# Optimization experiments

Measured on AMD Instinct MI355X. Metric: run time of the kernel, lower is better.

Reference implementation:

```python
import jax, jax.numpy as jnp
import numpy as np

HOURS = 24
SU, SL, TU, TL = 100.0, 0.0, 100.0, 0.0
N, M, L, E = 32, 128, 128, 128
T_DIM, U_DIM, L_DIM = 25, 2000, 10000


def setup_inputs() -> dict:
    key = jax.random.key(0)
    ks = jax.random.split(key, 18)
    s = 0.02
    full_seq = jax.random.randint(ks[0], (N, M), 1, L_DIM)
    time_seq = jax.random.randint(ks[1], (N, M), 1, 720)
    user = jax.random.randint(ks[2], (N,), 1, U_DIM)
    posneg = jax.random.randint(ks[3], (N, L), 1, L_DIM)
    traj_len = jax.random.randint(ks[4], (N,), 1, M + 1)
    mat1 = jax.random.uniform(ks[5], (N, M, M, 2), dtype=jnp.float32) * 100.0
    mat2 = jax.random.uniform(ks[6], (N, M, L), dtype=jnp.float32) * 100.0
    vec = jax.random.uniform(ks[7], (N, M), dtype=jnp.float32) * 100.0
    def tab(k, n):  # embedding table with padding_idx=0 zeroed
        return (jax.random.normal(k, (n, E), dtype=jnp.float32) * s).at[0].set(0.0)
    emb_t = tab(ks[8], T_DIM)
    emb_u = tab(ks[9], U_DIM)
    emb_loc = tab(ks[10], L_DIM)
    emb_sl = tab(ks[11], 2)
    emb_su = tab(ks[12], 2)
    emb_tl = tab(ks[13], 2)
    emb_tu = tab(ks[14], 2)
    Wq = jax.random.normal(ks[15], (E, E), dtype=jnp.float32) * s
    Wk = jax.random.normal(ks[16], (E, E), dtype=jnp.float32) * s
    Wv = jax.random.normal(ks[17], (E, E), dtype=jnp.float32) * s
    return dict(full_seq=full_seq, time_seq=time_seq, user=user, posneg=posneg,
                traj_len=traj_len, mat1=mat1, mat2=mat2, vec=vec,
                emb_t=emb_t, emb_u=emb_u, emb_loc=emb_loc,
                emb_sl=emb_sl, emb_su=emb_su, emb_tl=emb_tl, emb_tu=emb_tu,
                Wq=Wq, Wk=Wk, Wv=Wv)


def _interval(e_l, e_u, d, lo, hi):
    # (e_l*(hi-d) + e_u*(d-lo)) / (hi-lo); e_* are [...,E], d is [...]
    return (e_l * (hi - d)[..., None] + e_u * (d - lo)[..., None]) / (hi - lo)


def reference(full_seq, time_seq, user, posneg, traj_len, mat1, mat2, vec,
              emb_t, emb_u, emb_loc, emb_sl, emb_su, emb_tl, emb_tu, Wq, Wk, Wv):
    n, m = full_seq.shape
    tim = (time_seq - 1) % HOURS + 1
    joint = emb_t[tim] + emb_loc[full_seq] + emb_u[user][:, None, :]  # [N,M,E]

    # --- stage 1: self-attention with spatiotemporal relative bias ---
    delta_s, delta_t = mat1[..., 0], mat1[..., 1]  # [N,M,M]
    valid = (jnp.arange(m)[None, :] < traj_len[:, None]).astype(jnp.int32)  # [N,M]
    mask2d = valid[:, None, :] * valid[:, :, None]  # [N,M,M] in {0,1}
    delta = (_interval(emb_sl[mask2d], emb_su[mask2d], delta_s, SL, SU)
             + _interval(emb_tl[mask2d], emb_tu[mask2d], delta_t, TL, TU)).sum(-1)
    fmask = mask2d.astype(joint.dtype)
    q = joint @ Wq.T
    k = joint @ Wk.T
    v = joint @ Wv.T
    attn = jax.nn.softmax(jnp.einsum('bme,bne->bmn', q, k) + delta, axis=-1) * fmask
    self_attn = jnp.einsum('bmn,bne->bme', attn, v)  # [N,M,E]

    # --- stage 2: candidate attention ---
    mask1 = valid[:, :, None]  # [N,M,1]
    sp = _interval(emb_sl[mask1], emb_su[mask1], mat2, SL, SU)            # [N,M,L,E]
    tm = _interval(emb_tl[mask1], emb_tu[mask1], vec[:, :, None], TL, TU)  # [N,M,1,E]
    self_delta = jnp.swapaxes((sp + tm).sum(-1), -1, -2)  # [N,L,M]
    cand = emb_loc[posneg]  # [N,L,E]
    attn2 = jnp.einsum('ble,bme->blm', cand, self_attn) * self_delta
    return attn2.sum(-1)  # [N,L]
```

## Files before the change

### kernel.cpp

```cpp
#include <hip/hip_runtime.h>
#include <hip/hip_bf16.h>

#define HOURS 24
#define NB 32
#define MM 128
#define EE 128

typedef short bf16x8 __attribute__((ext_vector_type(8)));
typedef float f32x4 __attribute__((ext_vector_type(4)));

__device__ __forceinline__ unsigned short f2bfu(float f) {
    __hip_bfloat16 h = __float2bfloat16(f);
    return __builtin_bit_cast(unsigned short, h);
}
__device__ __forceinline__ unsigned int pack2(float a, float b) {
    return (unsigned int)f2bfu(a) | ((unsigned int)f2bfu(b) << 16);
}
__device__ __forceinline__ int swz8(int row, int unit) {
    return row * 128 + (((unit ^ (row & 7)) & 15) << 3);
}

__global__ __launch_bounds__(256) void k_qkv(
    const int* __restrict__ time_seq, const int* __restrict__ full_seq,
    const int* __restrict__ user,
    const float* __restrict__ emb_t, const float* __restrict__ emb_u,
    const float* __restrict__ emb_loc,
    const float* __restrict__ Wq, const float* __restrict__ Wk, const float* __restrict__ Wv,
    short* __restrict__ qws, short* __restrict__ kws, short* __restrict__ vtws)
{
    __shared__ alignas(16) short Wl[128 * 128];
    __shared__ alignas(16) short Jl[64 * 128];
    int b = blockIdx.y;
    int which = blockIdx.x >> 1;
    int half = blockIdx.x & 1;
    int m0 = half * 64;
    int tid = threadIdx.x;
    const float* W = (which == 0) ? Wq : (which == 1) ? Wk : Wv;

    const float4* W4 = (const float4*)W;
#pragma unroll
    for (int it = 0; it < 16; ++it) {
        int i4 = it * 256 + tid;
        float4 v = W4[i4];
        int n = i4 >> 5;
        int e = (i4 & 31) << 2;
        uint2 pk;
        pk.x = pack2(v.x, v.y);
        pk.y = pack2(v.z, v.w);
        *(uint2*)&Wl[swz8(n, e >> 3) + (e & 7)] = pk;
    }
    int uid = user[b];
    const float4* Eu4 = (const float4*)(emb_u + (size_t)uid * 128);
#pragma unroll
    for (int it = 0; it < 8; ++it) {
        int i4 = it * 256 + tid;
        int mm = i4 >> 5;
        int e = (i4 & 31) << 2;
        int m = m0 + mm;
        int t = time_seq[b * MM + m];
        int tim = (t - 1) % HOURS + 1;
        int loc = full_seq[b * MM + m];
        float4 a = ((const float4*)(emb_t + (size_t)tim * 128))[e >> 2];
        float4 c = ((const float4*)(emb_loc + (size_t)loc * 128))[e >> 2];
        float4 u = Eu4[e >> 2];
        uint2 pk;
        pk.x = pack2(a.x + c.x + u.x, a.y + c.y + u.y);
        pk.y = pack2(a.z + c.z + u.z, a.w + c.w + u.w);
        *(uint2*)&Jl[swz8(mm, e >> 3) + (e & 7)] = pk;
    }
    __syncthreads();

    int l = tid & 63, w = tid >> 6;
    int lr = l & 15, lg = l >> 4;

    if (which < 2) {
        bf16x8 af[2][4];
#pragma unroll
        for (int nt = 0; nt < 2; ++nt) {
            int n = (2 * w + nt) * 16 + lr;
#pragma unroll
            for (int kf = 0; kf < 4; ++kf)
                af[nt][kf] = *(const bf16x8*)&Wl[swz8(n, kf * 4 + lg)];
        }
        f32x4 acc[2][4];
#pragma unroll
        for (int nt = 0; nt < 2; ++nt)
#pragma unroll
            for (int mt = 0; mt < 4; ++mt) acc[nt][mt] = (f32x4){0.f, 0.f, 0.f, 0.f};
#pragma unroll
        for (int mt = 0; mt < 4; ++mt) {
            int m = mt * 16 + lr;
            bf16x8 bf[4];
#pragma unroll
            for (int kf = 0; kf < 4; ++kf)
                bf[kf] = *(const bf16x8*)&Jl[swz8(m, kf * 4 + lg)];
#pragma unroll
            for (int nt = 0; nt < 2; ++nt)
#pragma unroll
                for (int kf = 0; kf < 4; ++kf)
                    acc[nt][mt] = __builtin_amdgcn_mfma_f32_16x16x32_bf16(af[nt][kf], bf[kf], acc[nt][mt], 0, 0, 0);
        }
        short* outp = (which == 0) ? qws : kws;
#pragma unroll
        for (int nt = 0; nt < 2; ++nt)
#pragma unroll
            for (int mt = 0; mt < 4; ++mt) {
                int mg = m0 + mt * 16 + lr;
                int n0 = (2 * w + nt) * 16 + lg * 4;
                f32x4 a = acc[nt][mt];
                uint2 pk;
                pk.x = pack2(a[0], a[1]);
                pk.y = pack2(a[2], a[3]);
                *(uint2*)&outp[(size_t)(b * MM + mg) * EE + n0] = pk;
            }
    } else {
        bf16x8 bfr[2][4];
#pragma unroll
        for (int nt = 0; nt < 2; ++nt) {
            int n = (2 * w + nt) * 16 + lr;
#pragma unroll
            for (int kf = 0; kf < 4; ++kf)
                bfr[nt][kf] = *(const bf16x8*)&Wl[swz8(n, kf * 4 + lg)];
        }
        f32x4 acc[4][2];
#pragma unroll
        for (int mt = 0; mt < 4; ++mt)
#pragma unroll
            for (int nt = 0; nt < 2; ++nt) acc[mt][nt] = (f32x4){0.f, 0.f, 0.f, 0.f};
#pragma unroll
        for (int mt = 0; mt < 4; ++mt) {
            int m = mt * 16 + lr;
            bf16x8 af[4];
#pragma unroll
            for (int kf = 0; kf < 4; ++kf)
                af[kf] = *(const bf16x8*)&Jl[swz8(m, kf * 4 + lg)];
#pragma unroll
            for (int nt = 0; nt < 2; ++nt)
#pragma unroll
                for (int kf = 0; kf < 4; ++kf)
                    acc[mt][nt] = __builtin_amdgcn_mfma_f32_16x16x32_bf16(af[kf], bfr[nt][kf], acc[mt][nt], 0, 0, 0);
        }
#pragma unroll
        for (int mt = 0; mt < 4; ++mt)
#pragma unroll
            for (int nt = 0; nt < 2; ++nt) {
                int ng = (2 * w + nt) * 16 + lr;
                int mp = m0 + mt * 16 + lg * 4;
                f32x4 a = acc[mt][nt];
                uint2 pk;
                pk.x = pack2(a[0], a[1]);
                pk.y = pack2(a[2], a[3]);
                *(uint2*)&vtws[(size_t)(b * MM + ng) * MM + mp] = pk;
            }
    }
}

__global__ __launch_bounds__(256) void k_attn(
    const short* __restrict__ qws, const short* __restrict__ kws,
    const short* __restrict__ vtws,
    const float* __restrict__ mat1, const int* __restrict__ traj_len,
    const float* __restrict__ esl, const float* __restrict__ esu,
    const float* __restrict__ etl, const float* __restrict__ etu,
    short* __restrict__ saws)
{
    __shared__ alignas(16) short Kl[128 * 128];
    __shared__ alignas(16) short VTl[128 * 128];
    __shared__ alignas(16) short Pl[16 * 128];
    __shared__ alignas(16) float Sl[16][132];
    __shared__ float coef[8];

    int b = blockIdx.y;
    int chunk = blockIdx.x;
    int i0 = chunk * 16;
    int tid = threadIdx.x;
    int l = tid & 63, w = tid >> 6;
    int lr = l & 15, lg = l >> 4;
    int tl = traj_len[b];

    {
        const float* tb[4] = {esl, esu, etl, etu};
#pragma unroll
        for (int s = 0; s < 2; ++s) {
            int c = 2 * w + s;
            const float* t = tb[c >> 1];
            float v = t[(c & 1) * 128 + l] + t[(c & 1) * 128 + 64 + l];
#pragma unroll
            for (int off = 32; off >= 1; off >>= 1) v += __shfl_xor(v, off, 64);
            if (l == 0) coef[c] = v;
        }
    }
    const uint4* K4 = (const uint4*)(kws + (size_t)b * MM * EE);
    const uint4* VT4 = (const uint4*)(vtws + (size_t)b * MM * MM);
#pragma unroll
    for (int it = 0; it < 8; ++it) {
        int U = it * 256 + tid;
        int r = U >> 4, u = U & 15;
        *(uint4*)&Kl[swz8(r, u)] = K4[U];
    }
#pragma unroll
    for (int it = 0; it < 8; ++it) {
        int U = it * 256 + tid;
        int r = U >> 4, u = U & 15;
        *(uint4*)&VTl[swz8(r, u)] = VT4[U];
    }
    bf16x8 qf[4];
#pragma unroll
    for (int kf = 0; kf < 4; ++kf)
        qf[kf] = *(const bf16x8*)&qws[(size_t)(b * MM + i0 + lr) * EE + kf * 32 + lg * 8];
    __syncthreads();

    f32x4 accs[2];
#pragma unroll
    for (int t2 = 0; t2 < 2; ++t2) accs[t2] = (f32x4){0.f, 0.f, 0.f, 0.f};
#pragma unroll
    for (int t2 = 0; t2 < 2; ++t2) {
        int j = (2 * w + t2) * 16 + lr;
#pragma unroll
        for (int kf = 0; kf < 4; ++kf) {
            bf16x8 bf = *(const bf16x8*)&Kl[swz8(j, kf * 4 + lg)];
            accs[t2] = __builtin_amdgcn_mfma_f32_16x16x32_bf16(qf[kf], bf, accs[t2], 0, 0, 0);
        }
    }
#pragma unroll
    for (int t2 = 0; t2 < 2; ++t2) {
        int jc = (2 * w + t2) * 16 + lr;
#pragma unroll
        for (int r = 0; r < 4; ++r) Sl[lg * 4 + r][jc] = accs[t2][r];
    }
    __syncthreads();

    {
        int r16 = tid >> 4, u = tid & 15;
        int j0 = u * 8;
        int i = i0 + r16;
        int mi = (i < tl) ? 1 : 0;
        float c0_1 = coef[1] + coef[5];
        float c1_1 = (coef[3] - coef[1]) * 0.01f;
        float c2_1 = (coef[7] - coef[5]) * 0.01f;
        float c0_0 = coef[0] + coef[4];
        float c1_0 = (coef[2] - coef[0]) * 0.01f;
        float c2_0 = (coef[6] - coef[4]) * 0.01f;
        float4 s01 = *(float4*)&Sl[r16][j0];
        float4 s23 = *(float4*)&Sl[r16][j0 + 4];
        float sv[8] = {s01.x, s01.y, s01.z, s01.w, s23.x, s23.y, s23.z, s23.w};
        const float4* m14 = (const float4*)(mat1 + (size_t)(b * MM + i) * MM * 2 + j0 * 2);
        float4 d0 = m14[0], d1 = m14[1], d2 = m14[2], d3 = m14[3];
        float ds[8] = {d0.x, d0.z, d1.x, d1.z, d2.x, d2.z, d3.x, d3.z};
        float dt[8] = {d0.y, d0.w, d1.y, d1.w, d2.y, d2.w, d3.y, d3.w};
        float lgv[8];
        int mk[8];
#pragma unroll
        for (int jj = 0; jj < 8; ++jj) {
            int j = j0 + jj;
            mk[jj] = mi & ((j < tl) ? 1 : 0);
            float cc0 = mk[jj] ? c0_1 : c0_0;
            float cc1 = mk[jj] ? c1_1 : c1_0;
            float cc2 = mk[jj] ? c2_1 : c2_0;
            lgv[jj] = sv[jj] + cc0 + cc1 * ds[jj] + cc2 * dt[jj];
        }
        float mx = lgv[0];
#pragma unroll
        for (int jj = 1; jj < 8; ++jj) mx = fmaxf(mx, lgv[jj]);
#pragma unroll
        for (int off = 8; off >= 1; off >>= 1) mx = fmaxf(mx, __shfl_xor(mx, off, 64));
        float ee[8], sum = 0.f;
#pragma unroll
        for (int jj = 0; jj < 8; ++jj) { ee[jj] = __expf(lgv[jj] - mx); sum += ee[jj]; }
#pragma unroll
        for (int off = 8; off >= 1; off >>= 1) sum += __shfl_xor(sum, off, 64);
        float inv = 1.0f / sum;
        float p[8];
#pragma unroll
        for (int jj = 0; jj < 8; ++jj) p[jj] = ee[jj] * inv * (float)mk[jj];
        uint4 pk;
        pk.x = pack2(p[0], p[1]);
        pk.y = pack2(p[2], p[3]);
        pk.z = pack2(p[4], p[5]);
        pk.w = pack2(p[6], p[7]);
        *(uint4*)&Pl[swz8(r16, u)] = pk;
    }
    __syncthreads();

    bf16x8 bp[4];
#pragma unroll
    for (int kf = 0; kf < 4; ++kf)
        bp[kf] = *(const bf16x8*)&Pl[swz8(lr, kf * 4 + lg)];
    f32x4 accv[2];
#pragma unroll
    for (int t2 = 0; t2 < 2; ++t2) accv[t2] = (f32x4){0.f, 0.f, 0.f, 0.f};
#pragma unroll
    for (int t2 = 0; t2 < 2; ++t2) {
        int e = (2 * w + t2) * 16 + lr;
#pragma unroll
        for (int kf = 0; kf < 4; ++kf) {
            bf16x8 af = *(const bf16x8*)&VTl[swz8(e, kf * 4 + lg)];
            accv[t2] = __builtin_amdgcn_mfma_f32_16x16x32_bf16(af, bp[kf], accv[t2], 0, 0, 0);
        }
    }
#pragma unroll
    for (int t2 = 0; t2 < 2; ++t2) {
        int ig = i0 + lr;
        int e0 = (2 * w + t2) * 16 + lg * 4;
        f32x4 a = accv[t2];
        uint2 pk;
        pk.x = pack2(a[0], a[1]);
        pk.y = pack2(a[2], a[3]);
        *(uint2*)&saws[(size_t)(b * MM + ig) * EE + e0] = pk;
    }
}

__global__ __launch_bounds__(256) void k_final(
    const short* __restrict__ saws, const int* __restrict__ posneg,
    const float* __restrict__ emb_loc, const float* __restrict__ mat2,
    const float* __restrict__ vecg, const int* __restrict__ traj_len,
    const float* __restrict__ esl, const float* __restrict__ esu,
    const float* __restrict__ etl, const float* __restrict__ etu,
    float* __restrict__ outp)
{
    __shared__ alignas(16) short SAl[128 * 128];
    __shared__ alignas(16) short CAl[32 * 128];
    __shared__ alignas(16) float M2l[128 * 36];
    __shared__ float TMS[128];
    __shared__ float BSV[128];
    __shared__ float PART[2][32];
    __shared__ float coef[8];

    int b = blockIdx.y;
    int l0 = blockIdx.x * 32;
    int tid = threadIdx.x;
    int l = tid & 63, w = tid >> 6;
    int lr = l & 15, lg = l >> 4;
    int tl = traj_len[b];

    {
        const float* tb[4] = {esl, esu, etl, etu};
#pragma unroll
        for (int s = 0; s < 2; ++s) {
            int c = 2 * w + s;
            const float* t = tb[c >> 1];
            float v = t[(c & 1) * 128 + l] + t[(c & 1) * 128 + 64 + l];
#pragma unroll
            for (int off = 32; off >= 1; off >>= 1) v += __shfl_xor(v, off, 64);
            if (l == 0) coef[c] = v;
        }
    }
    const uint4* SA4 = (const uint4*)(saws + (size_t)b * MM * EE);
#pragma unroll
    for (int it = 0; it < 8; ++it) {
        int U = it * 256 + tid;
        int r = U >> 4, u = U & 15;
        *(uint4*)&SAl[swz8(r, u)] = SA4[U];
    }
#pragma unroll
    for (int it = 0; it < 4; ++it) {
        int i4 = it * 256 + tid;
        int lrow = i4 >> 5;
        int e = (i4 & 31) << 2;
        int p = posneg[b * MM + l0 + lrow];
        float4 v = ((const float4*)(emb_loc + (size_t)p * 128))[e >> 2];
        uint2 pk;
        pk.x = pack2(v.x, v.y);
        pk.y = pack2(v.z, v.w);
        *(uint2*)&CAl[swz8(lrow, e >> 3) + (e & 7)] = pk;
    }
#pragma unroll
    for (int it = 0; it < 4; ++it) {
        int i4 = it * 256 + tid;
        int m = i4 >> 3;
        int c = (i4 & 7) << 2;
        float4 v = ((const float4*)(mat2 + (size_t)(b * MM + m) * MM + l0))[c >> 2];
        *(float4*)&M2l[m * 36 + c] = v;
    }
    __syncthreads();

    if (tid < 128) {
        int vv = (tid < tl) ? 1 : 0;
        float ssl = vv ? coef[1] : coef[0];
        float ssu = vv ? coef[3] : coef[2];
        float stl = vv ? coef[5] : coef[4];
        float stu = vv ? coef[7] : coef[6];
        TMS[tid] = ssl + stl + (stu - stl) * 0.01f * vecg[b * MM + tid];
        BSV[tid] = (ssu - ssl) * 0.01f;
    }

    int ltile = w & 1, mhalf = w >> 1;
    bf16x8 ca[4];
#pragma unroll
    for (int kf = 0; kf < 4; ++kf)
        ca[kf] = *(const bf16x8*)&CAl[swz8(ltile * 16 + lr, kf * 4 + lg)];
    f32x4 acc[4];
#pragma unroll
    for (int mt = 0; mt < 4; ++mt) acc[mt] = (f32x4){0.f, 0.f, 0.f, 0.f};
#pragma unroll
    for (int mt = 0; mt < 4; ++mt) {
        int m = (mhalf * 4 + mt) * 16 + lr;
#pragma unroll
        for (int kf = 0; kf < 4; ++kf) {
            bf16x8 bf = *(const bf16x8*)&SAl[swz8(m, kf * 4 + lg)];
            acc[mt] = __builtin_amdgcn_mfma_f32_16x16x32_bf16(ca[kf], bf, acc[mt], 0, 0, 0);
        }
    }
    __syncthreads();

#pragma unroll
    for (int r = 0; r < 4; ++r) {
        int lrel = ltile * 16 + lg * 4 + r;
        float vs = 0.f;
#pragma unroll
        for (int mt = 0; mt < 4; ++mt) {
            int m = (mhalf * 4 + mt) * 16 + lr;
            vs += acc[mt][r] * (TMS[m] + BSV[m] * M2l[m * 36 + lrel]);
        }
#pragma unroll
        for (int off = 8; off >= 1; off >>= 1) vs += __shfl_xor(vs, off, 64);
        if (lr == 0) PART[mhalf][lrel] = vs;
    }
    __syncthreads();
    if (tid < 32) outp[b * MM + l0 + tid] = PART[0][tid] + PART[1][tid];
}

extern "C" void kernel_launch(void* const* d_in, const int* in_sizes, int n_in,
                              void* d_out, int out_size, void* d_ws, size_t ws_size,
                              hipStream_t stream) {
    const int* full_seq = (const int*)d_in[0];
    const int* time_seq = (const int*)d_in[1];
    const int* user     = (const int*)d_in[2];
    const int* posneg   = (const int*)d_in[3];
    const int* traj_len = (const int*)d_in[4];
    const float* mat1   = (const float*)d_in[5];
    const float* mat2   = (const float*)d_in[6];
    const float* vec    = (const float*)d_in[7];
    const float* emb_t  = (const float*)d_in[8];
    const float* emb_u  = (const float*)d_in[9];
    const float* emb_loc= (const float*)d_in[10];
    const float* emb_sl = (const float*)d_in[11];
    const float* emb_su = (const float*)d_in[12];
    const float* emb_tl = (const float*)d_in[13];
    const float* emb_tu = (const float*)d_in[14];
    const float* Wq     = (const float*)d_in[15];
    const float* Wk     = (const float*)d_in[16];
    const float* Wv     = (const float*)d_in[17];

    short* qws  = (short*)d_ws;
    short* kws  = qws + (size_t)NB * MM * EE;
    short* vtws = kws + (size_t)NB * MM * EE;
    short* saws = vtws + (size_t)NB * MM * EE;

    k_qkv<<<dim3(6, 32), 256, 0, stream>>>(time_seq, full_seq, user,
                                           emb_t, emb_u, emb_loc,
                                           Wq, Wk, Wv, qws, kws, vtws);
    k_attn<<<dim3(8, 32), 256, 0, stream>>>(qws, kws, vtws, mat1, traj_len,
                                            emb_sl, emb_su, emb_tl, emb_tu, saws);
    k_final<<<dim3(4, 32), 256, 0, stream>>>(saws, posneg, emb_loc, mat2, vec,
                                             traj_len, emb_sl, emb_su, emb_tl, emb_tu,
                                             (float*)d_out);
}
```

Before: 24.17 us.

## Fuse QKV, attention and candidate stages into one kernel per batch half

Replaces the three-kernel pipeline (QKV projection, self-attention, candidate attention) with a single 1024-thread kernel that runs per (batch, half of query rows) and keeps Q, K, V^T, probabilities and self-attention output in shared memory. Global workspace round trips and two kernel launches are removed. Each half block recomputes full K and V for its batch, and the two halves' partial candidate sums are combined with atomicAdd into an output zeroed by a memset. This duplicates some projection work, cuts the grid to 64 blocks, and uses large LDS per block.

```diff
diff --git a/kernel.cpp b/kernel.cpp
--- a/kernel.cpp
+++ b/kernel.cpp
@@ -2,7 +2,6 @@
 #include <hip/hip_bf16.h>
 
 #define HOURS 24
-#define NB 32
 #define MM 128
 #define EE 128
 
@@ -19,231 +18,188 @@
 __device__ __forceinline__ int swz8(int row, int unit) {
     return row * 128 + (((unit ^ (row & 7)) & 15) << 3);
 }
-
-__global__ __launch_bounds__(256) void k_qkv(
-    const int* __restrict__ time_seq, const int* __restrict__ full_seq,
-    const int* __restrict__ user,
+__device__ __forceinline__ bf16x8 load_w_frag(const float* base) {
+    float4 x = *(const float4*)base;
+    float4 y = *(const float4*)(base + 4);
+    union { unsigned int u[4]; bf16x8 v; } r;
+    r.u[0] = pack2(x.x, x.y); r.u[1] = pack2(x.z, x.w);
+    r.u[2] = pack2(y.x, y.y); r.u[3] = pack2(y.z, y.w);
+    return r.v;
+}
+
+#define MFMA(a, b, c) __builtin_amdgcn_mfma_f32_16x16x32_bf16(a, b, c, 0, 0, 0)
+
+__global__ __launch_bounds__(1024) void k_fused(
+    const int* __restrict__ full_seq, const int* __restrict__ time_seq,
+    const int* __restrict__ user, const int* __restrict__ posneg,
+    const int* __restrict__ traj_len,
+    const float* __restrict__ mat1, const float* __restrict__ mat2,
+    const float* __restrict__ vecg,
     const float* __restrict__ emb_t, const float* __restrict__ emb_u,
     const float* __restrict__ emb_loc,
-    const float* __restrict__ Wq, const float* __restrict__ Wk, const float* __restrict__ Wv,
-    short* __restrict__ qws, short* __restrict__ kws, short* __restrict__ vtws)
-{
-    __shared__ alignas(16) short Wl[128 * 128];
-    __shared__ alignas(16) short Jl[64 * 128];
-    int b = blockIdx.y;
-    int which = blockIdx.x >> 1;
-    int half = blockIdx.x & 1;
-    int m0 = half * 64;
-    int tid = threadIdx.x;
-    const float* W = (which == 0) ? Wq : (which == 1) ? Wk : Wv;
-
-    const float4* W4 = (const float4*)W;
-#pragma unroll
-    for (int it = 0; it < 16; ++it) {
-        int i4 = it * 256 + tid;
-        float4 v = W4[i4];
-        int n = i4 >> 5;
-        int e = (i4 & 31) << 2;
-        uint2 pk;
-        pk.x = pack2(v.x, v.y);
-        pk.y = pack2(v.z, v.w);
-        *(uint2*)&Wl[swz8(n, e >> 3) + (e & 7)] = pk;
-    }
-    int uid = user[b];
-    const float4* Eu4 = (const float4*)(emb_u + (size_t)uid * 128);
-#pragma unroll
-    for (int it = 0; it < 8; ++it) {
-        int i4 = it * 256 + tid;
-        int mm = i4 >> 5;
-        int e = (i4 & 31) << 2;
-        int m = m0 + mm;
-        int t = time_seq[b * MM + m];
-        int tim = (t - 1) % HOURS + 1;
-        int loc = full_seq[b * MM + m];
-        float4 a = ((const float4*)(emb_t + (size_t)tim * 128))[e >> 2];
-        float4 c = ((const float4*)(emb_loc + (size_t)loc * 128))[e >> 2];
-        float4 u = Eu4[e >> 2];
-        uint2 pk;
-        pk.x = pack2(a.x + c.x + u.x, a.y + c.y + u.y);
-        pk.y = pack2(a.z + c.z + u.z, a.w + c.w + u.w);
-        *(uint2*)&Jl[swz8(mm, e >> 3) + (e & 7)] = pk;
-    }
-    __syncthreads();
-
-    int l = tid & 63, w = tid >> 6;
-    int lr = l & 15, lg = l >> 4;
-
-    if (which < 2) {
-        bf16x8 af[2][4];
-#pragma unroll
-        for (int nt = 0; nt < 2; ++nt) {
-            int n = (2 * w + nt) * 16 + lr;
-#pragma unroll
-            for (int kf = 0; kf < 4; ++kf)
-                af[nt][kf] = *(const bf16x8*)&Wl[swz8(n, kf * 4 + lg)];
-        }
-        f32x4 acc[2][4];
-#pragma unroll
-        for (int nt = 0; nt < 2; ++nt)
-#pragma unroll
-            for (int mt = 0; mt < 4; ++mt) acc[nt][mt] = (f32x4){0.f, 0.f, 0.f, 0.f};
-#pragma unroll
-        for (int mt = 0; mt < 4; ++mt) {
-            int m = mt * 16 + lr;
-            bf16x8 bf[4];
-#pragma unroll
-            for (int kf = 0; kf < 4; ++kf)
-                bf[kf] = *(const bf16x8*)&Jl[swz8(m, kf * 4 + lg)];
-#pragma unroll
-            for (int nt = 0; nt < 2; ++nt)
-#pragma unroll
-                for (int kf = 0; kf < 4; ++kf)
-                    acc[nt][mt] = __builtin_amdgcn_mfma_f32_16x16x32_bf16(af[nt][kf], bf[kf], acc[nt][mt], 0, 0, 0);
-        }
-        short* outp = (which == 0) ? qws : kws;
-#pragma unroll
-        for (int nt = 0; nt < 2; ++nt)
-#pragma unroll
-            for (int mt = 0; mt < 4; ++mt) {
-                int mg = m0 + mt * 16 + lr;
-                int n0 = (2 * w + nt) * 16 + lg * 4;
-                f32x4 a = acc[nt][mt];
-                uint2 pk;
-                pk.x = pack2(a[0], a[1]);
-                pk.y = pack2(a[2], a[3]);
-                *(uint2*)&outp[(size_t)(b * MM + mg) * EE + n0] = pk;
-            }
-    } else {
-        bf16x8 bfr[2][4];
-#pragma unroll
-        for (int nt = 0; nt < 2; ++nt) {
-            int n = (2 * w + nt) * 16 + lr;
-#pragma unroll
-            for (int kf = 0; kf < 4; ++kf)
-                bfr[nt][kf] = *(const bf16x8*)&Wl[swz8(n, kf * 4 + lg)];
-        }
-        f32x4 acc[4][2];
-#pragma unroll
-        for (int mt = 0; mt < 4; ++mt)
-#pragma unroll
-            for (int nt = 0; nt < 2; ++nt) acc[mt][nt] = (f32x4){0.f, 0.f, 0.f, 0.f};
-#pragma unroll
-        for (int mt = 0; mt < 4; ++mt) {
-            int m = mt * 16 + lr;
-            bf16x8 af[4];
-#pragma unroll
-            for (int kf = 0; kf < 4; ++kf)
-                af[kf] = *(const bf16x8*)&Jl[swz8(m, kf * 4 + lg)];
-#pragma unroll
-            for (int nt = 0; nt < 2; ++nt)
-#pragma unroll
-                for (int kf = 0; kf < 4; ++kf)
-                    acc[mt][nt] = __builtin_amdgcn_mfma_f32_16x16x32_bf16(af[kf], bfr[nt][kf], acc[mt][nt], 0, 0, 0);
-        }
-#pragma unroll
-        for (int mt = 0; mt < 4; ++mt)
-#pragma unroll
-            for (int nt = 0; nt < 2; ++nt) {
-                int ng = (2 * w + nt) * 16 + lr;
-                int mp = m0 + mt * 16 + lg * 4;
-                f32x4 a = acc[mt][nt];
-                uint2 pk;
-                pk.x = pack2(a[0], a[1]);
-                pk.y = pack2(a[2], a[3]);
-                *(uint2*)&vtws[(size_t)(b * MM + ng) * MM + mp] = pk;
-            }
-    }
-}
-
-__global__ __launch_bounds__(256) void k_attn(
-    const short* __restrict__ qws, const short* __restrict__ kws,
-    const short* __restrict__ vtws,
-    const float* __restrict__ mat1, const int* __restrict__ traj_len,
     const float* __restrict__ esl, const float* __restrict__ esu,
     const float* __restrict__ etl, const float* __restrict__ etu,
-    short* __restrict__ saws)
+    const float* __restrict__ Wq, const float* __restrict__ Wk,
+    const float* __restrict__ Wv,
+    float* __restrict__ outp)
 {
-    __shared__ alignas(16) short Kl[128 * 128];
-    __shared__ alignas(16) short VTl[128 * 128];
-    __shared__ alignas(16) short Pl[16 * 128];
-    __shared__ alignas(16) float Sl[16][132];
-    __shared__ float coef[8];
-
-    int b = blockIdx.y;
-    int chunk = blockIdx.x;
-    int i0 = chunk * 16;
+    __shared__ alignas(16) short A_s[16896];
+    __shared__ alignas(16) short B_s[17408];
+    __shared__ alignas(16) short C_s[16384];
+    __shared__ alignas(16) short D_s[8192];
+    __shared__ alignas(16) short E_s[8192];
+    __shared__ float tms[64], bsv[64], coef[8];
+
+    int bid = blockIdx.x;
+    int b = bid >> 1, half = bid & 1;
+    int i0base = half * 64;
     int tid = threadIdx.x;
-    int l = tid & 63, w = tid >> 6;
+    int w = tid >> 6, l = tid & 63;
     int lr = l & 15, lg = l >> 4;
     int tl = traj_len[b];
 
-    {
-        const float* tb[4] = {esl, esu, etl, etu};
-#pragma unroll
-        for (int s = 0; s < 2; ++s) {
-            int c = 2 * w + s;
-            const float* t = tb[c >> 1];
-            float v = t[(c & 1) * 128 + l] + t[(c & 1) * 128 + 64 + l];
-#pragma unroll
-            for (int off = 32; off >= 1; off >>= 1) v += __shfl_xor(v, off, 64);
-            if (l == 0) coef[c] = v;
-        }
-    }
-    const uint4* K4 = (const uint4*)(kws + (size_t)b * MM * EE);
-    const uint4* VT4 = (const uint4*)(vtws + (size_t)b * MM * MM);
-#pragma unroll
-    for (int it = 0; it < 8; ++it) {
-        int U = it * 256 + tid;
-        int r = U >> 4, u = U & 15;
-        *(uint4*)&Kl[swz8(r, u)] = K4[U];
-    }
-#pragma unroll
-    for (int it = 0; it < 8; ++it) {
-        int U = it * 256 + tid;
-        int r = U >> 4, u = U & 15;
-        *(uint4*)&VTl[swz8(r, u)] = VT4[U];
-    }
-    bf16x8 qf[4];
-#pragma unroll
-    for (int kf = 0; kf < 4; ++kf)
-        qf[kf] = *(const bf16x8*)&qws[(size_t)(b * MM + i0 + lr) * EE + kf * 32 + lg * 8];
-    __syncthreads();
-
-    f32x4 accs[2];
-#pragma unroll
-    for (int t2 = 0; t2 < 2; ++t2) accs[t2] = (f32x4){0.f, 0.f, 0.f, 0.f};
-#pragma unroll
-    for (int t2 = 0; t2 < 2; ++t2) {
-        int j = (2 * w + t2) * 16 + lr;
-#pragma unroll
-        for (int kf = 0; kf < 4; ++kf) {
-            bf16x8 bf = *(const bf16x8*)&Kl[swz8(j, kf * 4 + lg)];
-            accs[t2] = __builtin_amdgcn_mfma_f32_16x16x32_bf16(qf[kf], bf, accs[t2], 0, 0, 0);
-        }
-    }
-#pragma unroll
-    for (int t2 = 0; t2 < 2; ++t2) {
-        int jc = (2 * w + t2) * 16 + lr;
-#pragma unroll
-        for (int r = 0; r < 4; ++r) Sl[lg * 4 + r][jc] = accs[t2][r];
-    }
-    __syncthreads();
-
-    {
-        int r16 = tid >> 4, u = tid & 15;
-        int j0 = u * 8;
-        int i = i0 + r16;
-        int mi = (i < tl) ? 1 : 0;
+    if (w >= 8) {
+        int c = w - 8;
+        const float* t = (c < 2) ? esl : (c < 4) ? esu : (c < 6) ? etl : etu;
+        int row = c & 1;
+        float v = t[row * 128 + l] + t[row * 128 + 64 + l];
+#pragma unroll
+        for (int off = 32; off >= 1; off >>= 1) v += __shfl_xor(v, off, 64);
+        if (l == 0) coef[c] = v;
+    }
+    {
+        int uid = user[b];
+        const float4* Eu4 = (const float4*)(emb_u + (size_t)uid * 128);
+#pragma unroll
+        for (int it = 0; it < 4; ++it) {
+            int u = it * 1024 + tid;
+            int mm = u >> 5;
+            int fq = u & 31;
+            int t = time_seq[b * MM + mm];
+            int tim = (t - 1) % HOURS + 1;
+            int loc = full_seq[b * MM + mm];
+            float4 a = ((const float4*)(emb_t + (size_t)tim * 128))[fq];
+            float4 c = ((const float4*)(emb_loc + (size_t)loc * 128))[fq];
+            float4 uu = Eu4[fq];
+            uint2 pk;
+            pk.x = pack2(a.x + c.x + uu.x, a.y + c.y + uu.y);
+            pk.y = pack2(a.z + c.z + uu.z, a.w + c.w + uu.w);
+            *(uint2*)&A_s[swz8(mm, fq >> 1) + (fq & 1) * 4] = pk;
+        }
+    }
+    __syncthreads();
+
+    if (w < 8) {
+        bf16x8 af[4];
+#pragma unroll
+        for (int kf = 0; kf < 4; ++kf)
+            af[kf] = load_w_frag(Wk + (size_t)(w * 16 + lr) * 128 + kf * 32 + lg * 8);
+        f32x4 acc[8];
+#pragma unroll
+        for (int mt = 0; mt < 8; ++mt) acc[mt] = (f32x4){0.f, 0.f, 0.f, 0.f};
+#pragma unroll
+        for (int mt = 0; mt < 8; ++mt)
+#pragma unroll
+            for (int kf = 0; kf < 4; ++kf) {
+                bf16x8 bf = *(const bf16x8*)&A_s[swz8(mt * 16 + lr, kf * 4 + lg)];
+                acc[mt] = MFMA(af[kf], bf, acc[mt]);
+            }
+        int n0 = w * 16 + lg * 4;
+#pragma unroll
+        for (int mt = 0; mt < 8; ++mt) {
+            int m = mt * 16 + lr;
+            uint2 pk;
+            pk.x = pack2(acc[mt][0], acc[mt][1]);
+            pk.y = pack2(acc[mt][2], acc[mt][3]);
+            *(uint2*)&B_s[swz8(m, n0 >> 3) + (n0 & 7)] = pk;
+        }
+    } else {
+        int w8 = w - 8;
+        bf16x8 aj[4];
+#pragma unroll
+        for (int kf = 0; kf < 4; ++kf)
+            aj[kf] = *(const bf16x8*)&A_s[swz8(w8 * 16 + lr, kf * 4 + lg)];
+#pragma unroll
+        for (int nt = 0; nt < 8; ++nt) {
+            f32x4 acc = (f32x4){0.f, 0.f, 0.f, 0.f};
+#pragma unroll
+            for (int kf = 0; kf < 4; ++kf) {
+                bf16x8 bw = load_w_frag(Wv + (size_t)(nt * 16 + lr) * 128 + kf * 32 + lg * 8);
+                acc = MFMA(aj[kf], bw, acc);
+            }
+            int n = nt * 16 + lr;
+#pragma unroll
+            for (int r = 0; r < 4; ++r) {
+                int m = w8 * 16 + lg * 4 + r;
+                C_s[swz8(n, m >> 3) + (m & 7)] = (short)f2bfu(acc[r]);
+            }
+        }
+    }
+    {
+        int nt = w & 7;
+        int mtb = (w < 8) ? 0 : 2;
+        bf16x8 aq[4];
+#pragma unroll
+        for (int kf = 0; kf < 4; ++kf)
+            aq[kf] = load_w_frag(Wq + (size_t)(nt * 16 + lr) * 128 + kf * 32 + lg * 8);
+#pragma unroll
+        for (int mi = 0; mi < 2; ++mi) {
+            int mt = mtb + mi;
+            f32x4 acc = (f32x4){0.f, 0.f, 0.f, 0.f};
+#pragma unroll
+            for (int kf = 0; kf < 4; ++kf) {
+                bf16x8 bf = *(const bf16x8*)&A_s[swz8(i0base + mt * 16 + lr, kf * 4 + lg)];
+                acc = MFMA(aq[kf], bf, acc);
+            }
+            int iloc = mt * 16 + lr;
+            int n0 = nt * 16 + lg * 4;
+            uint2 pk;
+            pk.x = pack2(acc[0], acc[1]);
+            pk.y = pack2(acc[2], acc[3]);
+            *(uint2*)&D_s[swz8(iloc, n0 >> 3) + (n0 & 7)] = pk;
+        }
+    }
+    __syncthreads();
+
+    float* Sf = (float*)A_s;
+    {
+        int chunk = w >> 2, sub = w & 3;
+        bf16x8 qf[4];
+#pragma unroll
+        for (int kf = 0; kf < 4; ++kf)
+            qf[kf] = *(const bf16x8*)&D_s[swz8(chunk * 16 + lr, kf * 4 + lg)];
+#pragma unroll
+        for (int t2 = 0; t2 < 2; ++t2) {
+            int jt = sub * 2 + t2;
+            f32x4 acc = (f32x4){0.f, 0.f, 0.f, 0.f};
+#pragma unroll
+            for (int kf = 0; kf < 4; ++kf) {
+                bf16x8 bf = *(const bf16x8*)&B_s[swz8(jt * 16 + lr, kf * 4 + lg)];
+                acc = MFMA(qf[kf], bf, acc);
+            }
+#pragma unroll
+            for (int r = 0; r < 4; ++r)
+                Sf[chunk * 2112 + (lg * 4 + r) * 132 + jt * 16 + lr] = acc[r];
+        }
+    }
+    __syncthreads();
+
+    {
+        int chunk = tid >> 8, t256 = tid & 255;
+        int r16 = t256 >> 4, u = t256 & 15, j0 = u * 8;
+        int ig = i0base + chunk * 16 + r16;
+        int mi = (ig < tl) ? 1 : 0;
         float c0_1 = coef[1] + coef[5];
         float c1_1 = (coef[3] - coef[1]) * 0.01f;
         float c2_1 = (coef[7] - coef[5]) * 0.01f;
         float c0_0 = coef[0] + coef[4];
         float c1_0 = (coef[2] - coef[0]) * 0.01f;
         float c2_0 = (coef[6] - coef[4]) * 0.01f;
-        float4 s01 = *(float4*)&Sl[r16][j0];
-        float4 s23 = *(float4*)&Sl[r16][j0 + 4];
+        const float* sb = &Sf[chunk * 2112 + r16 * 132 + j0];
+        float4 s01 = *(const float4*)sb;
+        float4 s23 = *(const float4*)(sb + 4);
         float sv[8] = {s01.x, s01.y, s01.z, s01.w, s23.x, s23.y, s23.z, s23.w};
-        const float4* m14 = (const float4*)(mat1 + (size_t)(b * MM + i) * MM * 2 + j0 * 2);
+        const float4* m14 = (const float4*)(mat1 + ((size_t)(b * MM + ig) * MM + j0) * 2);
         float4 d0 = m14[0], d1 = m14[1], d2 = m14[2], d3 = m14[3];
         float ds[8] = {d0.x, d0.z, d1.x, d1.z, d2.x, d2.z, d3.x, d3.z};
         float dt[8] = {d0.y, d0.w, d1.y, d1.w, d2.y, d2.w, d3.y, d3.w};
@@ -269,154 +225,109 @@
 #pragma unroll
         for (int off = 8; off >= 1; off >>= 1) sum += __shfl_xor(sum, off, 64);
         float inv = 1.0f / sum;
-        float p[8];
-#pragma unroll
-        for (int jj = 0; jj < 8; ++jj) p[jj] = ee[jj] * inv * (float)mk[jj];
         uint4 pk;
-        pk.x = pack2(p[0], p[1]);
-        pk.y = pack2(p[2], p[3]);
-        pk.z = pack2(p[4], p[5]);
-        pk.w = pack2(p[6], p[7]);
-        *(uint4*)&Pl[swz8(r16, u)] = pk;
-    }
-    __syncthreads();
-
-    bf16x8 bp[4];
-#pragma unroll
-    for (int kf = 0; kf < 4; ++kf)
-        bp[kf] = *(const bf16x8*)&Pl[swz8(lr, kf * 4 + lg)];
-    f32x4 accv[2];
-#pragma unroll
-    for (int t2 = 0; t2 < 2; ++t2) accv[t2] = (f32x4){0.f, 0.f, 0.f, 0.f};
-#pragma unroll
-    for (int t2 = 0; t2 < 2; ++t2) {
-        int e = (2 * w + t2) * 16 + lr;
-#pragma unroll
-        for (int kf = 0; kf < 4; ++kf) {
-            bf16x8 af = *(const bf16x8*)&VTl[swz8(e, kf * 4 + lg)];
-            accv[t2] = __builtin_amdgcn_mfma_f32_16x16x32_bf16(af, bp[kf], accv[t2], 0, 0, 0);
-        }
-    }
-#pragma unroll
-    for (int t2 = 0; t2 < 2; ++t2) {
-        int ig = i0 + lr;
-        int e0 = (2 * w + t2) * 16 + lg * 4;
-        f32x4 a = accv[t2];
-        uint2 pk;
-        pk.x = pack2(a[0], a[1]);
-        pk.y = pack2(a[2], a[3]);
-        *(uint2*)&saws[(size_t)(b * MM + ig) * EE + e0] = pk;
-    }
-}
-
-__global__ __launch_bounds__(256) void k_final(
-    const short* __restrict__ saws, const int* __restrict__ posneg,
-    const float* __restrict__ emb_loc, const float* __restrict__ mat2,
-    const float* __restrict__ vecg, const int* __restrict__ traj_len,
-    const float* __restrict__ esl, const float* __restrict__ esu,
-    const float* __restrict__ etl, const float* __restrict__ etu,
-    float* __restrict__ outp)
-{
-    __shared__ alignas(16) short SAl[128 * 128];
-    __shared__ alignas(16) short CAl[32 * 128];
-    __shared__ alignas(16) float M2l[128 * 36];
-    __shared__ float TMS[128];
-    __shared__ float BSV[128];
-    __shared__ float PART[2][32];
-    __shared__ float coef[8];
-
-    int b = blockIdx.y;
-    int l0 = blockIdx.x * 32;
-    int tid = threadIdx.x;
-    int l = tid & 63, w = tid >> 6;
-    int lr = l & 15, lg = l >> 4;
-    int tl = traj_len[b];
-
-    {
-        const float* tb[4] = {esl, esu, etl, etu};
-#pragma unroll
-        for (int s = 0; s < 2; ++s) {
-            int c = 2 * w + s;
-            const float* t = tb[c >> 1];
-            float v = t[(c & 1) * 128 + l] + t[(c & 1) * 128 + 64 + l];
-#pragma unroll
-            for (int off = 32; off >= 1; off >>= 1) v += __shfl_xor(v, off, 64);
-            if (l == 0) coef[c] = v;
-        }
-    }
-    const uint4* SA4 = (const uint4*)(saws + (size_t)b * MM * EE);
-#pragma unroll
-    for (int it = 0; it < 8; ++it) {
-        int U = it * 256 + tid;
-        int r = U >> 4, u = U & 15;
-        *(uint4*)&SAl[swz8(r, u)] = SA4[U];
-    }
-#pragma unroll
-    for (int it = 0; it < 4; ++it) {
-        int i4 = it * 256 + tid;
-        int lrow = i4 >> 5;
-        int e = (i4 & 31) << 2;
-        int p = posneg[b * MM + l0 + lrow];
-        float4 v = ((const float4*)(emb_loc + (size_t)p * 128))[e >> 2];
-        uint2 pk;
-        pk.x = pack2(v.x, v.y);
-        pk.y = pack2(v.z, v.w);
-        *(uint2*)&CAl[swz8(lrow, e >> 3) + (e & 7)] = pk;
-    }
-#pragma unroll
-    for (int it = 0; it < 4; ++it) {
-        int i4 = it * 256 + tid;
-        int m = i4 >> 3;
-        int c = (i4 & 7) << 2;
-        float4 v = ((const float4*)(mat2 + (size_t)(b * MM + m) * MM + l0))[c >> 2];
-        *(float4*)&M2l[m * 36 + c] = v;
-    }
-    __syncthreads();
-
-    if (tid < 128) {
-        int vv = (tid < tl) ? 1 : 0;
+        pk.x = pack2(ee[0] * inv * mk[0], ee[1] * inv * mk[1]);
+        pk.y = pack2(ee[2] * inv * mk[2], ee[3] * inv * mk[3]);
+        pk.z = pack2(ee[4] * inv * mk[4], ee[5] * inv * mk[5]);
+        pk.w = pack2(ee[6] * inv * mk[6], ee[7] * inv * mk[7]);
+        *(uint4*)&D_s[chunk * 2048 + swz8(r16, u)] = pk;
+    }
+    if (tid < 64) {
+        int mg = i0base + tid;
+        int vv = (mg < tl) ? 1 : 0;
         float ssl = vv ? coef[1] : coef[0];
         float ssu = vv ? coef[3] : coef[2];
         float stl = vv ? coef[5] : coef[4];
         float stu = vv ? coef[7] : coef[6];
-        TMS[tid] = ssl + stl + (stu - stl) * 0.01f * vecg[b * MM + tid];
-        BSV[tid] = (ssu - ssl) * 0.01f;
-    }
-
-    int ltile = w & 1, mhalf = w >> 1;
-    bf16x8 ca[4];
-#pragma unroll
-    for (int kf = 0; kf < 4; ++kf)
-        ca[kf] = *(const bf16x8*)&CAl[swz8(ltile * 16 + lr, kf * 4 + lg)];
-    f32x4 acc[4];
-#pragma unroll
-    for (int mt = 0; mt < 4; ++mt) acc[mt] = (f32x4){0.f, 0.f, 0.f, 0.f};
-#pragma unroll
-    for (int mt = 0; mt < 4; ++mt) {
-        int m = (mhalf * 4 + mt) * 16 + lr;
-#pragma unroll
-        for (int kf = 0; kf < 4; ++kf) {
-            bf16x8 bf = *(const bf16x8*)&SAl[swz8(m, kf * 4 + lg)];
-            acc[mt] = __builtin_amdgcn_mfma_f32_16x16x32_bf16(ca[kf], bf, acc[mt], 0, 0, 0);
-        }
-    }
-    __syncthreads();
-
-#pragma unroll
-    for (int r = 0; r < 4; ++r) {
-        int lrel = ltile * 16 + lg * 4 + r;
-        float vs = 0.f;
-#pragma unroll
-        for (int mt = 0; mt < 4; ++mt) {
-            int m = (mhalf * 4 + mt) * 16 + lr;
-            vs += acc[mt][r] * (TMS[m] + BSV[m] * M2l[m * 36 + lrel]);
-        }
-#pragma unroll
-        for (int off = 8; off >= 1; off >>= 1) vs += __shfl_xor(vs, off, 64);
-        if (lr == 0) PART[mhalf][lrel] = vs;
-    }
-    __syncthreads();
-    if (tid < 32) outp[b * MM + l0 + tid] = PART[0][tid] + PART[1][tid];
+        tms[tid] = ssl + stl + (stu - stl) * 0.01f * vecg[b * MM + mg];
+        bsv[tid] = (ssu - ssl) * 0.01f;
+    }
+    __syncthreads();
+
+    if (w < 8) {
+        int chunk = w >> 1, eh = w & 1;
+        bf16x8 bp[4];
+#pragma unroll
+        for (int kf = 0; kf < 4; ++kf)
+            bp[kf] = *(const bf16x8*)&D_s[chunk * 2048 + swz8(lr, kf * 4 + lg)];
+#pragma unroll
+        for (int e4 = 0; e4 < 4; ++e4) {
+            int et = eh * 4 + e4;
+            f32x4 acc = (f32x4){0.f, 0.f, 0.f, 0.f};
+#pragma unroll
+            for (int kf = 0; kf < 4; ++kf) {
+                bf16x8 af = *(const bf16x8*)&C_s[swz8(et * 16 + lr, kf * 4 + lg)];
+                acc = MFMA(af, bp[kf], acc);
+            }
+            int iloc = chunk * 16 + lr;
+            int e0 = et * 16 + lg * 4;
+            uint2 pk;
+            pk.x = pack2(acc[0], acc[1]);
+            pk.y = pack2(acc[2], acc[3]);
+            *(uint2*)&E_s[swz8(iloc, e0 >> 3) + (e0 & 7)] = pk;
+        }
+    } else {
+        int w8 = w - 8;
+#pragma unroll
+        for (int it = 0; it < 8; ++it) {
+            int u512 = it * 64 + l;
+            int rr = u512 >> 5, fq = u512 & 31;
+            int row = w8 * 16 + rr;
+            int p = posneg[b * MM + row];
+            float4 v = *(const float4*)(emb_loc + (size_t)p * 128 + fq * 4);
+            uint2 pk;
+            pk.x = pack2(v.x, v.y);
+            pk.y = pack2(v.z, v.w);
+            *(uint2*)&A_s[swz8(row, fq >> 1) + (fq & 1) * 4] = pk;
+        }
+        float* M2 = (float*)B_s;
+#pragma unroll
+        for (int it = 0; it < 4; ++it) {
+            int idx = it * 64 + l;
+            int mr = idx >> 5, fq = idx & 31;
+            int mloc = w8 * 8 + mr;
+            float4 v = *(const float4*)(mat2 + (size_t)(b * MM + i0base + mloc) * MM + fq * 4);
+            *(float4*)&M2[mloc * 136 + fq * 4] = v;
+        }
+    }
+    __syncthreads();
+
+    {
+        float* M2 = (float*)B_s;
+        int lt = w >> 1;
+        bf16x8 caf[4];
+#pragma unroll
+        for (int kf = 0; kf < 4; ++kf)
+            caf[kf] = *(const bf16x8*)&A_s[swz8(lt * 16 + lr, kf * 4 + lg)];
+        float vout[4] = {0.f, 0.f, 0.f, 0.f};
+#pragma unroll
+        for (int t2 = 0; t2 < 2; ++t2) {
+            int mt = (w & 1) * 2 + t2;
+            f32x4 acc = (f32x4){0.f, 0.f, 0.f, 0.f};
+#pragma unroll
+            for (int kf = 0; kf < 4; ++kf) {
+                bf16x8 bf = *(const bf16x8*)&E_s[swz8(mt * 16 + lr, kf * 4 + lg)];
+                acc = MFMA(caf[kf], bf, acc);
+            }
+            int mloc = mt * 16 + lr;
+            float wt = tms[mloc], wb = bsv[mloc];
+#pragma unroll
+            for (int r = 0; r < 4; ++r) {
+                int lidx = lt * 16 + lg * 4 + r;
+                vout[r] += acc[r] * (wt + wb * M2[mloc * 136 + lidx]);
+            }
+        }
+#pragma unroll
+        for (int r = 0; r < 4; ++r) {
+            float v = vout[r];
+            v += __shfl_xor(v, 8, 64);
+            v += __shfl_xor(v, 4, 64);
+            v += __shfl_xor(v, 2, 64);
+            v += __shfl_xor(v, 1, 64);
+            if (lr == 0)
+                atomicAdd(&outp[b * MM + lt * 16 + lg * 4 + r], v);
+        }
+    }
 }
 
 extern "C" void kernel_launch(void* const* d_in, const int* in_sizes, int n_in,
@@ -441,17 +352,9 @@
     const float* Wk     = (const float*)d_in[16];
     const float* Wv     = (const float*)d_in[17];
 
-    short* qws  = (short*)d_ws;
-    short* kws  = qws + (size_t)NB * MM * EE;
-    short* vtws = kws + (size_t)NB * MM * EE;
-    short* saws = vtws + (size_t)NB * MM * EE;
-
-    k_qkv<<<dim3(6, 32), 256, 0, stream>>>(time_seq, full_seq, user,
-                                           emb_t, emb_u, emb_loc,
-                                           Wq, Wk, Wv, qws, kws, vtws);
-    k_attn<<<dim3(8, 32), 256, 0, stream>>>(qws, kws, vtws, mat1, traj_len,
-                                            emb_sl, emb_su, emb_tl, emb_tu, saws);
-    k_final<<<dim3(4, 32), 256, 0, stream>>>(saws, posneg, emb_loc, mat2, vec,
-                                             traj_len, emb_sl, emb_su, emb_tl, emb_tu,
-                                             (float*)d_out);
-}
+    hipMemsetAsync(d_out, 0, (size_t)out_size * sizeof(float), stream);
+    k_fused<<<64, 1024, 0, stream>>>(full_seq, time_seq, user, posneg, traj_len,
+                                     mat1, mat2, vec, emb_t, emb_u, emb_loc,
+                                     emb_sl, emb_su, emb_tl, emb_tu,
+                                     Wq, Wk, Wv, (float*)d_out);
+}
```

After: 37.14 us. 53.6% more time.
